# Kernel tuning notes

Measured on AMD Instinct MI355X. Metric: run time of the kernel, lower is better.

Reference implementation:

```python
import jax, jax.numpy as jnp
import numpy as np

N = 50000
E = 800000
IN_C = 64
HID = 64
OUT_C = 64


def setup_inputs() -> dict:
    key = jax.random.key(0)
    ks = jax.random.split(key, 16)
    s = lambda fan_in: 1.0 / np.sqrt(fan_in)
    inp = {
        "h": jax.random.normal(ks[0], (N, IN_C), jnp.float32),
        "pos": jax.random.normal(ks[1], (N, 3), jnp.float32),
        "edge_index": jax.random.randint(ks[2], (2, E), 0, N, jnp.int64),
        # edge_mlp: Linear(2*IN_C+1, HID), SiLU, Linear(HID, HID), SiLU
        "We1": jax.random.normal(ks[3], (2 * IN_C + 1, HID), jnp.float32) * s(2 * IN_C + 1),
        "be1": jnp.zeros((HID,), jnp.float32),
        "We2": jax.random.normal(ks[4], (HID, HID), jnp.float32) * s(HID),
        "be2": jnp.zeros((HID,), jnp.float32),
        # coord_mlp: Linear(HID, HID), SiLU, Linear(HID, 1) with tiny init (xavier gain 1e-3)
        "Wc1": jax.random.normal(ks[5], (HID, HID), jnp.float32) * s(HID),
        "bc1": jnp.zeros((HID,), jnp.float32),
        "Wc2": jax.random.normal(ks[6], (HID, 1), jnp.float32) * (0.001 * s(HID)),
        "bc2": jnp.zeros((1,), jnp.float32),
        # node_mlp: Linear(IN_C+HID, HID), SiLU, Linear(HID, OUT_C)
        "Wn1": jax.random.normal(ks[7], (IN_C + HID, HID), jnp.float32) * s(IN_C + HID),
        "bn1": jnp.zeros((HID,), jnp.float32),
        "Wn2": jax.random.normal(ks[8], (HID, OUT_C), jnp.float32) * s(HID),
        "bn2": jnp.zeros((OUT_C,), jnp.float32),
    }
    return inp


def reference(h, pos, edge_index, We1, be1, We2, be2, Wc1, bc1, Wc2, bc2, Wn1, bn1, Wn2, bn2):
    row, col = edge_index[0], edge_index[1]
    n = h.shape[0]
    rel_pos = pos[row] - pos[col]                      # [E,3]
    dist_sq = jnp.sum(rel_pos * rel_pos, axis=-1, keepdims=True)  # [E,1]
    edge_input = jnp.concatenate([h[row], h[col], dist_sq], axis=-1)  # [E, 2*in+1]
    m = jax.nn.silu(edge_input @ We1 + be1)
    edge_msg = jax.nn.silu(m @ We2 + be2)              # [E,HID]
    # coordinate update
    cw = jax.nn.silu(edge_msg @ Wc1 + bc1) @ Wc2 + bc2  # [E,1]
    coord_agg = jax.ops.segment_sum(rel_pos * cw, row, num_segments=n)  # [N,3]
    pos_out = pos + coord_agg
    # message aggregation + node update
    msg_agg = jax.ops.segment_sum(edge_msg, row, num_segments=n)  # [N,HID]
    node_input = jnp.concatenate([h, msg_agg], axis=-1)
    h_out = jax.nn.silu(node_input @ Wn1 + bn1) @ Wn2 + bn2  # [N,OUT_C]
    return h_out, pos_out
```

## Files before the change

### kernel.cpp

```cpp
#include <hip/hip_runtime.h>


#define NN 50000
#define NE 800000
#define ETILE 12500

#define SBLK 250
#define SCHUNK 3200
#define NBUK 196
#define GHN 64000
#define SCAN_NB 63

typedef __attribute__((ext_vector_type(8))) short bf16x8;
typedef __attribute__((ext_vector_type(4))) short bf16x4;
typedef __attribute__((ext_vector_type(4))) float f32x4;

#define MFMA16(a, b, c) __builtin_amdgcn_mfma_f32_16x16x32_bf16(a, b, c, 0, 0, 0)

__device__ __forceinline__ unsigned short f2b(float x) {
    union { float f; unsigned u; } v; v.f = x;
    return (unsigned short)((v.u + 0x8000u) >> 16);
}
__device__ __forceinline__ float b2f(unsigned short b) {
    union { unsigned u; float f; } v; v.u = ((unsigned)b) << 16; return v.f;
}
__device__ __forceinline__ float silu_f(float x) {
    return x * __builtin_amdgcn_rcpf(1.0f + __expf(-x));
}



#define P1_A 250
#define P1_FRAG 10
#define P1_NPRE 782
#define P1_ZERO 200
#define P1_COPY 16
#define P1_FRAG0 (P1_A)
#define P1_NPRE0 (P1_A + P1_FRAG)
#define P1_ZERO0 (P1_NPRE0 + P1_NPRE)
#define P1_COPY0 (P1_ZERO0 + P1_ZERO)
#define K1_GRID (P1_COPY0 + P1_COPY)

__global__ __launch_bounds__(256, 4) void prep_kernel(
    const float* __restrict__ h, const float* __restrict__ pos,
    const float* __restrict__ be1,
    const float* __restrict__ We1, const float* __restrict__ We2,
    const float* __restrict__ Wc1, const float* __restrict__ Wn1,
    const float* __restrict__ Wn2, const int* __restrict__ ei,
    unsigned short* __restrict__ wfrag, int* __restrict__ gh,
    unsigned short* __restrict__ a1r, unsigned short* __restrict__ a1c,
    float* __restrict__ msg_agg, float* __restrict__ pos_out,
    float4* __restrict__ pos4)
{
    __shared__ __align__(16) unsigned short sH[64][72];
    __shared__ __align__(16) unsigned short sT[4][16][72];
    __shared__ int lh[256];
    const int b = blockIdx.x, tid = threadIdx.x;
    if (b < P1_A) {
        lh[tid] = 0;
        __syncthreads();
        const int base = b * SCHUNK;
        for (int i = base + tid; i < base + SCHUNK; i += 256)
            atomicAdd(&lh[ei[i] >> 8], 1);
        __syncthreads();
        gh[tid * SBLK + b] = lh[tid];
    } else if (b < P1_NPRE0) {
        const int lane = tid & 63, w = tid >> 6;
        const int li = lane & 15, lg = lane >> 4;
        const int f = (b - P1_FRAG0) * 4 + w;
        const float* W; int g;
        if (f < 8)       { W = We2; g = f; }
        else if (f < 16) { W = Wc1; g = f - 8; }
        else if (f < 32) { W = Wn1; g = f - 16; }
        else             { W = Wn2; g = f - 32; }
        const int ks = g >> 2, ni = g & 3;
        const int n = ni * 16 + li, kb = ks * 32 + (lg << 3);
        bf16x8 v;
#pragma unroll
        for (int j = 0; j < 8; ++j) v[j] = (short)f2b(W[(kb + j) * 64 + n]);
        *(bf16x8*)(wfrag + (size_t)f * 512 + lane * 8) = v;
    } else if (b < P1_ZERO0) {
        const int lane = tid & 63, w = tid >> 6;
        const int li = lane & 15, lg = lane >> 4;
        const int t = b - P1_NPRE0;
        const int c4 = lane & 15, rsub = lane >> 4;
#pragma unroll
        for (int pass = 0; pass < 4; ++pass) {
            const int n_loc = w * 16 + pass * 4 + rsub;
            const int n = t * 64 + n_loc;
            float4 hv = make_float4(0.f, 0.f, 0.f, 0.f);
            if (n < NN) hv = *(const float4*)&h[(size_t)n * 64 + c4 * 4];
            bf16x4 hp;
            hp[0] = (short)f2b(hv.x); hp[1] = (short)f2b(hv.y);
            hp[2] = (short)f2b(hv.z); hp[3] = (short)f2b(hv.w);
            *(bf16x4*)&sH[n_loc][c4 * 4] = hp;
        }
        float be1v[4];
#pragma unroll
        for (int ni = 0; ni < 4; ++ni) be1v[ni] = be1[ni * 16 + li];

#pragma unroll
        for (int half = 0; half < 2; ++half) {
            unsigned short* out = half ? a1c : a1r;
            f32x4 acc[4];
#pragma unroll
            for (int ni = 0; ni < 4; ++ni) acc[ni] = (f32x4)(0.0f);
#pragma unroll
            for (int ks = 0; ks < 2; ++ks) {
                const bf16x8 afr = *(const bf16x8*)&sH[w * 16 + li][ks * 32 + (lg << 3)];
#pragma unroll
                for (int ni = 0; ni < 4; ++ni) {
                    const float* Wp = We1 +
                        (size_t)(half * 64 + ks * 32 + (lg << 3)) * 64 + ni * 16 + li;
                    bf16x8 bfr;
#pragma unroll
                    for (int j = 0; j < 8; ++j) bfr[j] = (short)f2b(Wp[(size_t)j * 64]);
                    acc[ni] = MFMA16(afr, bfr, acc[ni]);
                }
            }
#pragma unroll
            for (int ni = 0; ni < 4; ++ni)
#pragma unroll
                for (int reg = 0; reg < 4; ++reg)
                    sT[w][lg * 4 + reg][ni * 16 + li] =
                        f2b(acc[ni][reg] + (half ? 0.f : be1v[ni]));
#pragma unroll
            for (int pass = 0; pass < 2; ++pass) {
                const int rr = pass * 8 + (lane >> 3);
                const int n = t * 64 + w * 16 + rr;
                const bf16x8 v = *(const bf16x8*)&sT[w][rr][(lane & 7) * 8];
                if (n < NN) *(bf16x8*)&out[(size_t)n * 64 + (lane & 7) * 8] = v;
            }
        }
    } else if (b < P1_COPY0) {
        float4* dst = (float4*)msg_agg;
        int i = (b - P1_ZERO0) * 256 + tid;
        for (; i < NN * 16; i += P1_ZERO * 256) dst[i] = make_float4(0.f, 0.f, 0.f, 0.f);
    } else {
        if (b == P1_COPY0 && tid < 128) gh[GHN + tid] = 0;
        int i = (b - P1_COPY0) * 256 + tid;
        for (; i < 37500 + NN; i += P1_COPY * 256) {
            if (i < 37500) {
                ((float4*)pos_out)[i] = ((const float4*)pos)[i];
            } else {
                const int n = i - 37500;
                pos4[n] = make_float4(pos[3 * n], pos[3 * n + 1], pos[3 * n + 2], 0.f);
            }
        }
    }
}


__global__ __launch_bounds__(1024) void scan_kernel(int* __restrict__ cur,
                                                    int* __restrict__ aux) {
    __shared__ int wsum[16];
    __shared__ int s_prefix;
    const int b = blockIdx.x, t = threadIdx.x;
    const int g = b * 1024 + t;
    const int lane = t & 63, wid = t >> 6;
    const int v = (g < GHN) ? cur[g] : 0;
    int inc = v;
#pragma unroll
    for (int d = 1; d < 64; d <<= 1) {
        const int o = __shfl_up(inc, d, 64);
        if (lane >= d) inc += o;
    }
    if (lane == 63) wsum[wid] = inc;
    __syncthreads();
    if (t < 16) {
        int x = wsum[t];
#pragma unroll
        for (int d = 1; d < 16; d <<= 1) {
            const int o = __shfl_up(x, d, 16);
            if (t >= d) x += o;
        }
        wsum[t] = x;
    }
    __syncthreads();
    const int block_excl_w = (wid == 0) ? 0 : wsum[wid - 1];
    const int ex_in_block = block_excl_w + inc - v;
    if (t == 0) {
        __hip_atomic_store(&aux[b], wsum[15], __ATOMIC_RELAXED, __HIP_MEMORY_SCOPE_AGENT);
        __hip_atomic_store(&aux[SCAN_NB + b], 1, __ATOMIC_RELEASE, __HIP_MEMORY_SCOPE_AGENT);
    }
    if (t < 64) {
        int s = 0;
        if (t < b) {
            while (__hip_atomic_load(&aux[SCAN_NB + t], __ATOMIC_ACQUIRE,
                                     __HIP_MEMORY_SCOPE_AGENT) == 0) {
                __builtin_amdgcn_s_sleep(2);
            }
            s = __hip_atomic_load(&aux[t], __ATOMIC_RELAXED, __HIP_MEMORY_SCOPE_AGENT);
        }
#pragma unroll
        for (int m = 1; m < 64; m <<= 1) s += __shfl_xor(s, m, 64);
        if (t == 0) s_prefix = s;
    }
    __syncthreads();
    if (g < GHN) cur[g] = s_prefix + ex_in_block;
}


__global__ __launch_bounds__(256) void scat_kernel(const int* __restrict__ ei,
                                                   const int* __restrict__ gh,
                                                   int2* __restrict__ sorted_rc) {
    __shared__ int off[256];
    const int b = blockIdx.x, t = threadIdx.x;
    off[t] = gh[t * SBLK + b];
    __syncthreads();
    const int base = b * SCHUNK;
    for (int i = base + t; i < base + SCHUNK; i += 256) {
        const int r = ei[i];
        const int c = ei[NE + i];
        const int p = atomicAdd(&off[r >> 8], 1);
        sorted_rc[p] = make_int2(r, c);
    }
}


__global__ __launch_bounds__(256) void bsort_kernel(const int* __restrict__ gh,
                                                    int2* __restrict__ sorted_rc) {
    __shared__ int h2[256];
    __shared__ int sc[256];
    __shared__ int off2[256];
    __shared__ __align__(16) int2 stage[4096];
    const int k = blockIdx.x, t = threadIdx.x;
    const int start = gh[k * SBLK];
    const int end   = gh[(k + 1) * SBLK];
    for (int cb = start; cb < end; cb += 4096) {
        const int cnt = min(4096, end - cb);
        h2[t] = 0;
        __syncthreads();
        int2 le[16];
        int nloc = 0;
#pragma unroll
        for (int jj = 0; jj < 16; ++jj) {
            const int j = jj * 256 + t;
            if (j < cnt) {
                const int2 e = sorted_rc[cb + j];
                le[jj] = e;
                atomicAdd(&h2[e.x & 255], 1);
                nloc = jj + 1;
            }
        }
        __syncthreads();
        sc[t] = h2[t];
        __syncthreads();
        for (int d = 1; d < 256; d <<= 1) {
            const int v = (t >= d) ? sc[t - d] : 0;
            __syncthreads();
            sc[t] += v;
            __syncthreads();
        }
        off2[t] = sc[t] - h2[t];
        __syncthreads();
#pragma unroll
        for (int jj = 0; jj < 16; ++jj) {
            if (jj < nloc) {
                const int rank = atomicAdd(&off2[le[jj].x & 255], 1);
                stage[rank] = le[jj];
            }
        }
        __syncthreads();
        for (int j = t; j < cnt; j += 256) sorted_rc[cb + j] = stage[j];
        __syncthreads();
    }
}


__global__ __launch_bounds__(256, 6) void egnn_edge_kernel(
    const float4* __restrict__ pos4, const int2* __restrict__ sorted_rc,
    const unsigned short* __restrict__ a1r, const unsigned short* __restrict__ a1c,
    const float* __restrict__ We1,
    const unsigned short* __restrict__ wfrag,
    const float* __restrict__ be2, const float* __restrict__ bc1,
    const float* __restrict__ Wc2, const float* __restrict__ bc2,
    float* __restrict__ msg_agg, float* __restrict__ pos_out)
{
    __shared__ __align__(16) unsigned short sA[64][80];
    __shared__ __align__(8) int2 srce[64];
    __shared__ __align__(16) float4 sdr[64];
    __shared__ float scw[64];

    const int tid = threadIdx.x;
    const int lane = tid & 63, w = tid >> 6;
    const int li = lane & 15, lg = lane >> 4;
    const int tile = blockIdx.x;
    const int e0 = w * 16;

    if (lane < 16) {
        const int e = e0 + lane;
        const int2 rc = sorted_rc[tile * 64 + e];
        const float4 pr = pos4[rc.x];
        const float4 pc = pos4[rc.y];
        const float rx = pr.x - pc.x, ry = pr.y - pc.y, rz = pr.z - pc.z;
        srce[e] = rc;
        sdr[e] = make_float4(rx, ry, rz, rx * rx + ry * ry + rz * rz);
    }

    const int c8 = lane & 7;
    const int eo = lane >> 3;

    float w1d8[8];
    {
        const float* wd = We1 + 128 * 64 + c8 * 8;
        const float4 wa = *(const float4*)wd;
        const float4 wb = *(const float4*)(wd + 4);
        w1d8[0] = wa.x; w1d8[1] = wa.y; w1d8[2] = wa.z; w1d8[3] = wa.w;
        w1d8[4] = wb.x; w1d8[5] = wb.y; w1d8[6] = wb.z; w1d8[7] = wb.w;
    }
    float be2v[4], bc1v[4], wc2v[4];
#pragma unroll
    for (int ni = 0; ni < 4; ++ni) {
        be2v[ni] = be2[ni * 16 + li];
        bc1v[ni] = bc1[ni * 16 + li];
        wc2v[ni] = Wc2[ni * 16 + li];
    }
    const float bc2s = bc2[0];

#pragma unroll
    for (int hh = 0; hh < 2; ++hh) {
        const int e = e0 + hh * 8 + eo;
        const int2 rc = srce[e];
        const float dv = sdr[e].w;
        const bf16x8 ar = *(const bf16x8*)(a1r + (size_t)rc.x * 64 + c8 * 8);
        const bf16x8 ac = *(const bf16x8*)(a1c + (size_t)rc.y * 64 + c8 * 8);
        bf16x8 out;
#pragma unroll
        for (int j = 0; j < 8; ++j) {
            const float m = b2f((unsigned short)ar[j]) + b2f((unsigned short)ac[j])
                          + dv * w1d8[j];
            out[j] = (short)f2b(silu_f(m));
        }
        *(bf16x8*)&sA[e][c8 * 8] = out;
    }

    f32x4 acc[4];
#pragma unroll
    for (int ni = 0; ni < 4; ++ni) acc[ni] = (f32x4)(0.0f);
#pragma unroll
    for (int ks = 0; ks < 2; ++ks) {
        const bf16x8 af = *(const bf16x8*)&sA[e0 + li][ks * 32 + (lg << 3)];
#pragma unroll
        for (int ni = 0; ni < 4; ++ni) {
            const bf16x8 bf = *(const bf16x8*)(wfrag + (size_t)(ks * 4 + ni) * 512 + lane * 8);
            acc[ni] = MFMA16(af, bf, acc[ni]);
        }
    }

#pragma unroll
    for (int ni = 0; ni < 4; ++ni)
#pragma unroll
        for (int reg = 0; reg < 4; ++reg)
            sA[e0 + lg * 4 + reg][ni * 16 + li] = f2b(silu_f(acc[ni][reg] + be2v[ni]));

    {
        float macc = 0.0f;
        int pr = srce[e0].x;
#pragma unroll
        for (int j = 0; j < 16; ++j) {
            const int re = srce[e0 + j].x;
            if (re != pr) {
                atomicAdd(&msg_agg[(size_t)pr * 64 + lane], macc);
                macc = 0.0f;
                pr = re;
            }
            macc += b2f(sA[e0 + j][lane]);
        }
        atomicAdd(&msg_agg[(size_t)pr * 64 + lane], macc);
    }

    f32x4 a3[4];
#pragma unroll
    for (int ni = 0; ni < 4; ++ni) a3[ni] = (f32x4)(0.0f);
#pragma unroll
    for (int ks = 0; ks < 2; ++ks) {
        const bf16x8 af = *(const bf16x8*)&sA[e0 + li][ks * 32 + (lg << 3)];
#pragma unroll
        for (int ni = 0; ni < 4; ++ni) {
            const bf16x8 bf = *(const bf16x8*)(wfrag + (size_t)(8 + ks * 4 + ni) * 512 + lane * 8);
            a3[ni] = MFMA16(af, bf, a3[ni]);
        }
    }

    float sv[4];
#pragma unroll
    for (int reg = 0; reg < 4; ++reg) {
        float s = 0.0f;
#pragma unroll
        for (int ni = 0; ni < 4; ++ni)
            s += silu_f(a3[ni][reg] + bc1v[ni]) * wc2v[ni];
        sv[reg] = s;
    }
#pragma unroll
    for (int m = 1; m < 16; m <<= 1)
#pragma unroll
        for (int reg = 0; reg < 4; ++reg) sv[reg] += __shfl_xor(sv[reg], m, 64);
    if (li == 0) {
        float4 cv = make_float4(sv[0] + bc2s, sv[1] + bc2s, sv[2] + bc2s, sv[3] + bc2s);
        *(float4*)&scw[e0 + lg * 4] = cv;
    }
    __syncthreads();

    if (tid < 64) {
        const float4 dr = sdr[tid];
        const int r_e = srce[tid].x;
        const float cw = scw[tid];
        float vx = dr.x * cw, vy = dr.y * cw, vz = dr.z * cw;
#pragma unroll
        for (int d = 1; d < 64; d <<= 1) {
            const float ox = __shfl_up(vx, d, 64);
            const float oy = __shfl_up(vy, d, 64);
            const float oz = __shfl_up(vz, d, 64);
            const int   orr = __shfl_up(r_e, d, 64);
            const bool add = (tid >= d) && (orr == r_e);
            vx += add ? ox : 0.0f;
            vy += add ? oy : 0.0f;
            vz += add ? oz : 0.0f;
        }
        const int rnext = __shfl_down(r_e, 1, 64);
        const bool last = (tid == 63) || (rnext != r_e);
        if (last) {
            atomicAdd(&pos_out[r_e * 3 + 0], vx);
            atomicAdd(&pos_out[r_e * 3 + 1], vy);
            atomicAdd(&pos_out[r_e * 3 + 2], vz);
        }
    }
}


__global__ __launch_bounds__(256, 4) void node_kernel(
    const float* __restrict__ h, const float* __restrict__ msg_agg,
    const unsigned short* __restrict__ wfrag,
    const float* __restrict__ bn1, const float* __restrict__ bn2,
    float* __restrict__ h_out)
{
    __shared__ __align__(16) unsigned short sA[64][136];
    const int tid = threadIdx.x;
    const int lane = tid & 63, w = tid >> 6;
    const int t = blockIdx.x;
    const int li = lane & 15, lg = lane >> 4;

    float bn1v[4], bn2v[4];
#pragma unroll
    for (int ni = 0; ni < 4; ++ni) {
        bn1v[ni] = bn1[ni * 16 + li];
        bn2v[ni] = bn2[ni * 16 + li];
    }

#pragma unroll
    for (int pass = 0; pass < 8; ++pass) {
        const int idx = pass * 64 + lane;
        const int n_loc = w * 16 + (idx >> 5);
        const int c4 = idx & 31;
        const int n = t * 64 + n_loc;
        float4 v = make_float4(0.f, 0.f, 0.f, 0.f);
        if (n < NN) {
            const float* src = (c4 < 16) ? &h[(size_t)n * 64 + c4 * 4]
                                         : &msg_agg[(size_t)n * 64 + (c4 - 16) * 4];
            v = *(const float4*)src;
        }
        bf16x4 p;
        p[0] = (short)f2b(v.x); p[1] = (short)f2b(v.y);
        p[2] = (short)f2b(v.z); p[3] = (short)f2b(v.w);
        *(bf16x4*)&sA[n_loc][c4 * 4] = p;
    }

    f32x4 acc[4];
#pragma unroll
    for (int ni = 0; ni < 4; ++ni) acc[ni] = (f32x4)(0.0f);
#pragma unroll
    for (int ks = 0; ks < 4; ++ks) {
        const bf16x8 afr = *(const bf16x8*)&sA[w * 16 + li][ks * 32 + (lg << 3)];
#pragma unroll
        for (int ni = 0; ni < 4; ++ni) {
            const bf16x8 bfr = *(const bf16x8*)(wfrag + (size_t)(16 + ks * 4 + ni) * 512 + lane * 8);
            acc[ni] = MFMA16(afr, bfr, acc[ni]);
        }
    }
#pragma unroll
    for (int ni = 0; ni < 4; ++ni)
#pragma unroll
        for (int reg = 0; reg < 4; ++reg)
            sA[w * 16 + lg * 4 + reg][ni * 16 + li] = f2b(silu_f(acc[ni][reg] + bn1v[ni]));

    f32x4 a2[4];
#pragma unroll
    for (int ni = 0; ni < 4; ++ni) a2[ni] = (f32x4)(0.0f);
#pragma unroll
    for (int ks = 0; ks < 2; ++ks) {
        const bf16x8 afr = *(const bf16x8*)&sA[w * 16 + li][ks * 32 + (lg << 3)];
#pragma unroll
        for (int ni = 0; ni < 4; ++ni) {
            const bf16x8 bfr = *(const bf16x8*)(wfrag + (size_t)(32 + ks * 4 + ni) * 512 + lane * 8);
            a2[ni] = MFMA16(afr, bfr, a2[ni]);
        }
    }
#pragma unroll
    for (int ni = 0; ni < 4; ++ni)
#pragma unroll
        for (int reg = 0; reg < 4; ++reg) {
            const int n = t * 64 + w * 16 + lg * 4 + reg;
            if (n < NN) h_out[(size_t)n * 64 + ni * 16 + li] = a2[ni][reg] + bn2v[ni];
        }
}


extern "C" void kernel_launch(void* const* d_in, const int* in_sizes, int n_in,
                              void* d_out, int out_size, void* d_ws, size_t ws_size,
                              hipStream_t stream) {
    const float* h   = (const float*)d_in[0];
    const float* pos = (const float*)d_in[1];
    const int*   ei  = (const int*)d_in[2];
    const float* We1 = (const float*)d_in[3];
    const float* be1 = (const float*)d_in[4];
    const float* We2 = (const float*)d_in[5];
    const float* be2 = (const float*)d_in[6];
    const float* Wc1 = (const float*)d_in[7];
    const float* bc1 = (const float*)d_in[8];
    const float* Wc2 = (const float*)d_in[9];
    const float* bc2 = (const float*)d_in[10];
    const float* Wn1 = (const float*)d_in[11];
    const float* bn1 = (const float*)d_in[12];
    const float* Wn2 = (const float*)d_in[13];
    const float* bn2 = (const float*)d_in[14];

    unsigned short* a1r   = (unsigned short*)d_ws;
    unsigned short* a1c   = a1r + (size_t)NN * 64;
    unsigned short* wfrag = a1c + (size_t)NN * 64;
    int2* sorted_rc = (int2*)(wfrag + 40 * 512);
    int*  gh        = (int*)(sorted_rc + NE);
    float4* pos4    = (float4*)(gh + GHN + 128);

    float* msg_agg = (float*)d_out;
    float* pos_out = msg_agg + (size_t)NN * 64;

    prep_kernel<<<K1_GRID, 256, 0, stream>>>(h, pos, be1, We1, We2, Wc1, Wn1, Wn2,
                                             ei, wfrag, gh, a1r, a1c,
                                             msg_agg, pos_out, pos4);
    scan_kernel<<<SCAN_NB, 1024, 0, stream>>>(gh, gh + GHN);
    scat_kernel<<<SBLK, 256, 0, stream>>>(ei, gh, sorted_rc);
    bsort_kernel<<<NBUK, 256, 0, stream>>>(gh, sorted_rc);
    egnn_edge_kernel<<<ETILE, 256, 0, stream>>>(pos4, sorted_rc, a1r, a1c, We1, wfrag,
                                                be2, bc1, Wc2, bc2, msg_agg, pos_out);
    node_kernel<<<782, 256, 0, stream>>>(h, msg_agg, wfrag, bn1, bn2, msg_agg);
}
```

Measured before the change: 199.6 us.

## Fuse scan, scatter, bucket sort and node precompute into one kernel with flag sync

```diff
diff --git a/kernel.cpp b/kernel.cpp
--- a/kernel.cpp
+++ b/kernel.cpp
@@ -32,28 +32,22 @@
 
 #define P1_A 250
 #define P1_FRAG 10
-#define P1_NPRE 782
 #define P1_ZERO 200
 #define P1_COPY 16
 #define P1_FRAG0 (P1_A)
-#define P1_NPRE0 (P1_A + P1_FRAG)
-#define P1_ZERO0 (P1_NPRE0 + P1_NPRE)
+#define P1_ZERO0 (P1_FRAG0 + P1_FRAG)
 #define P1_COPY0 (P1_ZERO0 + P1_ZERO)
 #define K1_GRID (P1_COPY0 + P1_COPY)
 
 __global__ __launch_bounds__(256, 4) void prep_kernel(
-    const float* __restrict__ h, const float* __restrict__ pos,
-    const float* __restrict__ be1,
-    const float* __restrict__ We1, const float* __restrict__ We2,
-    const float* __restrict__ Wc1, const float* __restrict__ Wn1,
-    const float* __restrict__ Wn2, const int* __restrict__ ei,
+    const float* __restrict__ pos,
+    const float* __restrict__ We2, const float* __restrict__ Wc1,
+    const float* __restrict__ Wn1, const float* __restrict__ Wn2,
+    const int* __restrict__ ei,
     unsigned short* __restrict__ wfrag, int* __restrict__ gh,
-    unsigned short* __restrict__ a1r, unsigned short* __restrict__ a1c,
     float* __restrict__ msg_agg, float* __restrict__ pos_out,
     float4* __restrict__ pos4)
 {
-    __shared__ __align__(16) unsigned short sH[64][72];
-    __shared__ __align__(16) unsigned short sT[4][16][72];
     __shared__ int lh[256];
     const int b = blockIdx.x, tid = threadIdx.x;
     if (b < P1_A) {
@@ -64,7 +58,7 @@
             atomicAdd(&lh[ei[i] >> 8], 1);
         __syncthreads();
         gh[tid * SBLK + b] = lh[tid];
-    } else if (b < P1_NPRE0) {
+    } else if (b < P1_ZERO0) {
         const int lane = tid & 63, w = tid >> 6;
         const int li = lane & 15, lg = lane >> 4;
         const int f = (b - P1_FRAG0) * 4 + w;
@@ -79,59 +73,6 @@
 #pragma unroll
         for (int j = 0; j < 8; ++j) v[j] = (short)f2b(W[(kb + j) * 64 + n]);
         *(bf16x8*)(wfrag + (size_t)f * 512 + lane * 8) = v;
-    } else if (b < P1_ZERO0) {
-        const int lane = tid & 63, w = tid >> 6;
-        const int li = lane & 15, lg = lane >> 4;
-        const int t = b - P1_NPRE0;
-        const int c4 = lane & 15, rsub = lane >> 4;
-#pragma unroll
-        for (int pass = 0; pass < 4; ++pass) {
-            const int n_loc = w * 16 + pass * 4 + rsub;
-            const int n = t * 64 + n_loc;
-            float4 hv = make_float4(0.f, 0.f, 0.f, 0.f);
-            if (n < NN) hv = *(const float4*)&h[(size_t)n * 64 + c4 * 4];
-            bf16x4 hp;
-            hp[0] = (short)f2b(hv.x); hp[1] = (short)f2b(hv.y);
-            hp[2] = (short)f2b(hv.z); hp[3] = (short)f2b(hv.w);
-            *(bf16x4*)&sH[n_loc][c4 * 4] = hp;
-        }
-        float be1v[4];
-#pragma unroll
-        for (int ni = 0; ni < 4; ++ni) be1v[ni] = be1[ni * 16 + li];
-
-#pragma unroll
-        for (int half = 0; half < 2; ++half) {
-            unsigned short* out = half ? a1c : a1r;
-            f32x4 acc[4];
-#pragma unroll
-            for (int ni = 0; ni < 4; ++ni) acc[ni] = (f32x4)(0.0f);
-#pragma unroll
-            for (int ks = 0; ks < 2; ++ks) {
-                const bf16x8 afr = *(const bf16x8*)&sH[w * 16 + li][ks * 32 + (lg << 3)];
-#pragma unroll
-                for (int ni = 0; ni < 4; ++ni) {
-                    const float* Wp = We1 +
-                        (size_t)(half * 64 + ks * 32 + (lg << 3)) * 64 + ni * 16 + li;
-                    bf16x8 bfr;
-#pragma unroll
-                    for (int j = 0; j < 8; ++j) bfr[j] = (short)f2b(Wp[(size_t)j * 64]);
-                    acc[ni] = MFMA16(afr, bfr, acc[ni]);
-                }
-            }
-#pragma unroll
-            for (int ni = 0; ni < 4; ++ni)
-#pragma unroll
-                for (int reg = 0; reg < 4; ++reg)
-                    sT[w][lg * 4 + reg][ni * 16 + li] =
-                        f2b(acc[ni][reg] + (half ? 0.f : be1v[ni]));
-#pragma unroll
-            for (int pass = 0; pass < 2; ++pass) {
-                const int rr = pass * 8 + (lane >> 3);
-                const int n = t * 64 + w * 16 + rr;
-                const bf16x8 v = *(const bf16x8*)&sT[w][rr][(lane & 7) * 8];
-                if (n < NN) *(bf16x8*)&out[(size_t)n * 64 + (lane & 7) * 8] = v;
-            }
-        }
     } else if (b < P1_COPY0) {
         float4* dst = (float4*)msg_agg;
         int i = (b - P1_ZERO0) * 256 + tid;
@@ -151,119 +92,200 @@
 }
 
 
-__global__ __launch_bounds__(1024) void scan_kernel(int* __restrict__ cur,
-                                                    int* __restrict__ aux) {
-    __shared__ int wsum[16];
-    __shared__ int s_prefix;
-    const int b = blockIdx.x, t = threadIdx.x;
-    const int g = b * 1024 + t;
-    const int lane = t & 63, wid = t >> 6;
-    const int v = (g < GHN) ? cur[g] : 0;
-    int inc = v;
-#pragma unroll
-    for (int d = 1; d < 64; d <<= 1) {
-        const int o = __shfl_up(inc, d, 64);
-        if (lane >= d) inc += o;
-    }
-    if (lane == 63) wsum[wid] = inc;
-    __syncthreads();
-    if (t < 16) {
-        int x = wsum[t];
-#pragma unroll
-        for (int d = 1; d < 16; d <<= 1) {
-            const int o = __shfl_up(x, d, 16);
-            if (t >= d) x += o;
-        }
-        wsum[t] = x;
-    }
-    __syncthreads();
-    const int block_excl_w = (wid == 0) ? 0 : wsum[wid - 1];
-    const int ex_in_block = block_excl_w + inc - v;
-    if (t == 0) {
-        __hip_atomic_store(&aux[b], wsum[15], __ATOMIC_RELAXED, __HIP_MEMORY_SCOPE_AGENT);
-        __hip_atomic_store(&aux[SCAN_NB + b], 1, __ATOMIC_RELEASE, __HIP_MEMORY_SCOPE_AGENT);
-    }
-    if (t < 64) {
-        int s = 0;
-        if (t < b) {
-            while (__hip_atomic_load(&aux[SCAN_NB + t], __ATOMIC_ACQUIRE,
-                                     __HIP_MEMORY_SCOPE_AGENT) == 0) {
-                __builtin_amdgcn_s_sleep(2);
-            }
-            s = __hip_atomic_load(&aux[t], __ATOMIC_RELAXED, __HIP_MEMORY_SCOPE_AGENT);
-        }
-#pragma unroll
-        for (int m = 1; m < 64; m <<= 1) s += __shfl_xor(s, m, 64);
-        if (t == 0) s_prefix = s;
-    }
-    __syncthreads();
-    if (g < GHN) cur[g] = s_prefix + ex_in_block;
-}
-
-
-__global__ __launch_bounds__(256) void scat_kernel(const int* __restrict__ ei,
-                                                   const int* __restrict__ gh,
-                                                   int2* __restrict__ sorted_rc) {
-    __shared__ int off[256];
-    const int b = blockIdx.x, t = threadIdx.x;
-    off[t] = gh[t * SBLK + b];
-    __syncthreads();
-    const int base = b * SCHUNK;
-    for (int i = base + t; i < base + SCHUNK; i += 256) {
-        const int r = ei[i];
-        const int c = ei[NE + i];
-        const int p = atomicAdd(&off[r >> 8], 1);
-        sorted_rc[p] = make_int2(r, c);
-    }
-}
-
-
-__global__ __launch_bounds__(256) void bsort_kernel(const int* __restrict__ gh,
-                                                    int2* __restrict__ sorted_rc) {
-    __shared__ int h2[256];
-    __shared__ int sc[256];
-    __shared__ int off2[256];
-    __shared__ __align__(16) int2 stage[4096];
-    const int k = blockIdx.x, t = threadIdx.x;
-    const int start = gh[k * SBLK];
-    const int end   = gh[(k + 1) * SBLK];
-    for (int cb = start; cb < end; cb += 4096) {
-        const int cnt = min(4096, end - cb);
-        h2[t] = 0;
-        __syncthreads();
-        int2 le[16];
-        int nloc = 0;
-#pragma unroll
-        for (int jj = 0; jj < 16; ++jj) {
-            const int j = jj * 256 + t;
-            if (j < cnt) {
-                const int2 e = sorted_rc[cb + j];
-                le[jj] = e;
-                atomicAdd(&h2[e.x & 255], 1);
-                nloc = jj + 1;
-            }
-        }
-        __syncthreads();
-        sc[t] = h2[t];
-        __syncthreads();
-        for (int d = 1; d < 256; d <<= 1) {
-            const int v = (t >= d) ? sc[t - d] : 0;
+#define K2_SCAN 63
+#define K2_SCAT0 63
+#define K2_NPRE0 313
+#define K2_BS0 1095
+#define K2_GRID 1291
+
+union K2Smem {
+    struct { unsigned short sH[64][72]; unsigned short sT[4][16][72]; } np;
+    struct { int wsum[4]; int prefix; } scn;
+    struct { int off[256]; } st;
+    struct { int2 stage[4096]; int h2[256]; int sc2[256]; int off2[256]; } bs;
+};
+
+__global__ __launch_bounds__(256) void sort_fused_kernel(
+    const float* __restrict__ h, const float* __restrict__ be1,
+    const float* __restrict__ We1, const int* __restrict__ ei,
+    int* __restrict__ gh,
+    unsigned short* __restrict__ a1r, unsigned short* __restrict__ a1c,
+    int2* __restrict__ sorted_rc)
+{
+    __shared__ __align__(16) K2Smem smem;
+    const int b = blockIdx.x, tid = threadIdx.x;
+    int* aux = gh + GHN;
+    const int lane = tid & 63, wid = tid >> 6;
+
+    if (b < K2_SCAN) {
+        const int base4 = (b * 256 + tid) * 4;
+        int vv[4];
+#pragma unroll
+        for (int i = 0; i < 4; ++i) {
+            const int idx = base4 + i;
+            vv[i] = (idx < GHN) ? gh[idx] : 0;
+        }
+        const int s = vv[0] + vv[1] + vv[2] + vv[3];
+        int inc = s;
+#pragma unroll
+        for (int d = 1; d < 64; d <<= 1) {
+            const int o = __shfl_up(inc, d, 64);
+            if (lane >= d) inc += o;
+        }
+        if (lane == 63) smem.scn.wsum[wid] = inc;
+        __syncthreads();
+        if (tid == 0) {
+            int run = 0;
+#pragma unroll
+            for (int i = 0; i < 4; ++i) {
+                const int tmp = smem.scn.wsum[i]; smem.scn.wsum[i] = run; run += tmp;
+            }
+            __hip_atomic_store(&aux[b], run, __ATOMIC_RELAXED, __HIP_MEMORY_SCOPE_AGENT);
+            __hip_atomic_store(&aux[SCAN_NB + b], 1, __ATOMIC_RELEASE, __HIP_MEMORY_SCOPE_AGENT);
+        }
+        __syncthreads();
+        const int thr_excl = smem.scn.wsum[wid] + inc - s;
+        if (tid < 64) {
+            int s2 = 0;
+            if (tid < b) {
+                while (__hip_atomic_load(&aux[SCAN_NB + tid], __ATOMIC_ACQUIRE,
+                                         __HIP_MEMORY_SCOPE_AGENT) == 0) {
+                    __builtin_amdgcn_s_sleep(2);
+                }
+                s2 = __hip_atomic_load(&aux[tid], __ATOMIC_RELAXED, __HIP_MEMORY_SCOPE_AGENT);
+            }
+#pragma unroll
+            for (int m = 1; m < 64; m <<= 1) s2 += __shfl_xor(s2, m, 64);
+            if (tid == 0) smem.scn.prefix = s2;
+        }
+        __syncthreads();
+        int run = smem.scn.prefix + thr_excl;
+#pragma unroll
+        for (int i = 0; i < 4; ++i) {
+            const int idx = base4 + i;
+            if (idx < GHN) gh[idx] = run;
+            run += vv[i];
+        }
+        __syncthreads();
+        if (tid == 0)
+            __hip_atomic_fetch_add(&aux[126], 1, __ATOMIC_RELEASE, __HIP_MEMORY_SCOPE_AGENT);
+    } else if (b < K2_NPRE0) {
+        while (__hip_atomic_load(&aux[126], __ATOMIC_ACQUIRE,
+                                 __HIP_MEMORY_SCOPE_AGENT) != K2_SCAN) {
+            __builtin_amdgcn_s_sleep(2);
+        }
+        const int bb = b - K2_SCAT0;
+        smem.st.off[tid] = gh[tid * SBLK + bb];
+        __syncthreads();
+        const int base = bb * SCHUNK;
+        for (int i = base + tid; i < base + SCHUNK; i += 256) {
+            const int r = ei[i];
+            const int c = ei[NE + i];
+            const int p = atomicAdd(&smem.st.off[r >> 8], 1);
+            sorted_rc[p] = make_int2(r, c);
+        }
+        __syncthreads();
+        if (tid == 0)
+            __hip_atomic_fetch_add(&aux[127], 1, __ATOMIC_RELEASE, __HIP_MEMORY_SCOPE_AGENT);
+    } else if (b < K2_BS0) {
+        const int li = lane & 15, lg = lane >> 4;
+        const int w = wid;
+        const int t = b - K2_NPRE0;
+        const int c4 = lane & 15, rsub = lane >> 4;
+#pragma unroll
+        for (int pass = 0; pass < 4; ++pass) {
+            const int n_loc = w * 16 + pass * 4 + rsub;
+            const int n = t * 64 + n_loc;
+            float4 hv = make_float4(0.f, 0.f, 0.f, 0.f);
+            if (n < NN) hv = *(const float4*)&h[(size_t)n * 64 + c4 * 4];
+            bf16x4 hp;
+            hp[0] = (short)f2b(hv.x); hp[1] = (short)f2b(hv.y);
+            hp[2] = (short)f2b(hv.z); hp[3] = (short)f2b(hv.w);
+            *(bf16x4*)&smem.np.sH[n_loc][c4 * 4] = hp;
+        }
+        float be1v[4];
+#pragma unroll
+        for (int ni = 0; ni < 4; ++ni) be1v[ni] = be1[ni * 16 + li];
+
+#pragma unroll
+        for (int half = 0; half < 2; ++half) {
+            unsigned short* out = half ? a1c : a1r;
+            f32x4 acc[4];
+#pragma unroll
+            for (int ni = 0; ni < 4; ++ni) acc[ni] = (f32x4)(0.0f);
+#pragma unroll
+            for (int ks = 0; ks < 2; ++ks) {
+                const bf16x8 afr = *(const bf16x8*)&smem.np.sH[w * 16 + li][ks * 32 + (lg << 3)];
+#pragma unroll
+                for (int ni = 0; ni < 4; ++ni) {
+                    const float* Wp = We1 +
+                        (size_t)(half * 64 + ks * 32 + (lg << 3)) * 64 + ni * 16 + li;
+                    bf16x8 bfr;
+#pragma unroll
+                    for (int j = 0; j < 8; ++j) bfr[j] = (short)f2b(Wp[(size_t)j * 64]);
+                    acc[ni] = MFMA16(afr, bfr, acc[ni]);
+                }
+            }
+#pragma unroll
+            for (int ni = 0; ni < 4; ++ni)
+#pragma unroll
+                for (int reg = 0; reg < 4; ++reg)
+                    smem.np.sT[w][lg * 4 + reg][ni * 16 + li] =
+                        f2b(acc[ni][reg] + (half ? 0.f : be1v[ni]));
+#pragma unroll
+            for (int pass = 0; pass < 2; ++pass) {
+                const int rr = pass * 8 + (lane >> 3);
+                const int n = t * 64 + w * 16 + rr;
+                const bf16x8 v = *(const bf16x8*)&smem.np.sT[w][rr][(lane & 7) * 8];
+                if (n < NN) *(bf16x8*)&out[(size_t)n * 64 + (lane & 7) * 8] = v;
+            }
+        }
+    } else {
+        while (__hip_atomic_load(&aux[127], __ATOMIC_ACQUIRE,
+                                 __HIP_MEMORY_SCOPE_AGENT) != SBLK) {
+            __builtin_amdgcn_s_sleep(2);
+        }
+        const int k = b - K2_BS0, t = tid;
+        const int start = gh[k * SBLK];
+        const int end   = gh[(k + 1) * SBLK];
+        for (int cb = start; cb < end; cb += 4096) {
+            const int cnt = min(4096, end - cb);
+            smem.bs.h2[t] = 0;
             __syncthreads();
-            sc[t] += v;
+            int2 le[16];
+            int nloc = 0;
+#pragma unroll
+            for (int jj = 0; jj < 16; ++jj) {
+                const int j = jj * 256 + t;
+                if (j < cnt) {
+                    const int2 e = sorted_rc[cb + j];
+                    le[jj] = e;
+                    atomicAdd(&smem.bs.h2[e.x & 255], 1);
+                    nloc = jj + 1;
+                }
+            }
             __syncthreads();
-        }
-        off2[t] = sc[t] - h2[t];
-        __syncthreads();
-#pragma unroll
-        for (int jj = 0; jj < 16; ++jj) {
-            if (jj < nloc) {
-                const int rank = atomicAdd(&off2[le[jj].x & 255], 1);
-                stage[rank] = le[jj];
-            }
-        }
-        __syncthreads();
-        for (int j = t; j < cnt; j += 256) sorted_rc[cb + j] = stage[j];
-        __syncthreads();
+            smem.bs.sc2[t] = smem.bs.h2[t];
+            __syncthreads();
+            for (int d = 1; d < 256; d <<= 1) {
+                const int v = (t >= d) ? smem.bs.sc2[t - d] : 0;
+                __syncthreads();
+                smem.bs.sc2[t] += v;
+                __syncthreads();
+            }
+            smem.bs.off2[t] = smem.bs.sc2[t] - smem.bs.h2[t];
+            __syncthreads();
+#pragma unroll
+            for (int jj = 0; jj < 16; ++jj) {
+                if (jj < nloc) {
+                    const int rank = atomicAdd(&smem.bs.off2[le[jj].x & 255], 1);
+                    smem.bs.stage[rank] = le[jj];
+                }
+            }
+            __syncthreads();
+            for (int j = t; j < cnt; j += 256) sorted_rc[cb + j] = smem.bs.stage[j];
+            __syncthreads();
+        }
     }
 }
 
@@ -535,12 +557,10 @@
     float* msg_agg = (float*)d_out;
     float* pos_out = msg_agg + (size_t)NN * 64;
 
-    prep_kernel<<<K1_GRID, 256, 0, stream>>>(h, pos, be1, We1, We2, Wc1, Wn1, Wn2,
-                                             ei, wfrag, gh, a1r, a1c,
-                                             msg_agg, pos_out, pos4);
-    scan_kernel<<<SCAN_NB, 1024, 0, stream>>>(gh, gh + GHN);
-    scat_kernel<<<SBLK, 256, 0, stream>>>(ei, gh, sorted_rc);
-    bsort_kernel<<<NBUK, 256, 0, stream>>>(gh, sorted_rc);
+    prep_kernel<<<K1_GRID, 256, 0, stream>>>(pos, We2, Wc1, Wn1, Wn2, ei,
+                                             wfrag, gh, msg_agg, pos_out, pos4);
+    sort_fused_kernel<<<K2_GRID, 256, 0, stream>>>(h, be1, We1, ei, gh,
+                                                   a1r, a1c, sorted_rc);
     egnn_edge_kernel<<<ETILE, 256, 0, stream>>>(pos4, sorted_rc, a1r, a1c, We1, wfrag,
                                                 be2, bc1, Wc2, bc2, msg_agg, pos_out);
     node_kernel<<<782, 256, 0, stream>>>(h, msg_agg, wfrag, bn1, bn2, msg_agg);
```

New measurement: 401.4 us. 2.01x slower.

## Fuse scan and scatter kernels with device-wide flag sync; raise edge kernel occupancy

Applied to the files above, without the earlier changes.

```diff
diff --git a/kernel.cpp b/kernel.cpp
--- a/kernel.cpp
+++ b/kernel.cpp
@@ -151,69 +151,87 @@
 }
 
 
-__global__ __launch_bounds__(1024) void scan_kernel(int* __restrict__ cur,
-                                                    int* __restrict__ aux) {
-    __shared__ int wsum[16];
+#define SS_SCAN 63
+#define SS_GRID 313
+
+__global__ __launch_bounds__(256) void scanscat_kernel(
+    const int* __restrict__ ei, int* __restrict__ gh,
+    int2* __restrict__ sorted_rc)
+{
+    __shared__ int wsum[4];
     __shared__ int s_prefix;
-    const int b = blockIdx.x, t = threadIdx.x;
-    const int g = b * 1024 + t;
-    const int lane = t & 63, wid = t >> 6;
-    const int v = (g < GHN) ? cur[g] : 0;
-    int inc = v;
-#pragma unroll
-    for (int d = 1; d < 64; d <<= 1) {
-        const int o = __shfl_up(inc, d, 64);
-        if (lane >= d) inc += o;
-    }
-    if (lane == 63) wsum[wid] = inc;
-    __syncthreads();
-    if (t < 16) {
-        int x = wsum[t];
-#pragma unroll
-        for (int d = 1; d < 16; d <<= 1) {
-            const int o = __shfl_up(x, d, 16);
-            if (t >= d) x += o;
-        }
-        wsum[t] = x;
-    }
-    __syncthreads();
-    const int block_excl_w = (wid == 0) ? 0 : wsum[wid - 1];
-    const int ex_in_block = block_excl_w + inc - v;
-    if (t == 0) {
-        __hip_atomic_store(&aux[b], wsum[15], __ATOMIC_RELAXED, __HIP_MEMORY_SCOPE_AGENT);
-        __hip_atomic_store(&aux[SCAN_NB + b], 1, __ATOMIC_RELEASE, __HIP_MEMORY_SCOPE_AGENT);
-    }
-    if (t < 64) {
-        int s = 0;
-        if (t < b) {
-            while (__hip_atomic_load(&aux[SCAN_NB + t], __ATOMIC_ACQUIRE,
-                                     __HIP_MEMORY_SCOPE_AGENT) == 0) {
-                __builtin_amdgcn_s_sleep(2);
-            }
-            s = __hip_atomic_load(&aux[t], __ATOMIC_RELAXED, __HIP_MEMORY_SCOPE_AGENT);
-        }
-#pragma unroll
-        for (int m = 1; m < 64; m <<= 1) s += __shfl_xor(s, m, 64);
-        if (t == 0) s_prefix = s;
-    }
-    __syncthreads();
-    if (g < GHN) cur[g] = s_prefix + ex_in_block;
-}
-
-
-__global__ __launch_bounds__(256) void scat_kernel(const int* __restrict__ ei,
-                                                   const int* __restrict__ gh,
-                                                   int2* __restrict__ sorted_rc) {
     __shared__ int off[256];
-    const int b = blockIdx.x, t = threadIdx.x;
-    off[t] = gh[t * SBLK + b];
-    __syncthreads();
-    const int base = b * SCHUNK;
-    for (int i = base + t; i < base + SCHUNK; i += 256) {
-        const int r = ei[i];
-        const int c = ei[NE + i];
-        const int p = atomicAdd(&off[r >> 8], 1);
-        sorted_rc[p] = make_int2(r, c);
+    const int b = blockIdx.x, tid = threadIdx.x;
+    int* aux = gh + GHN;
+    const int lane = tid & 63, wid = tid >> 6;
+
+    if (b < SS_SCAN) {
+        const int base4 = (b * 256 + tid) * 4;
+        int vv[4];
+#pragma unroll
+        for (int i = 0; i < 4; ++i) {
+            const int idx = base4 + i;
+            vv[i] = (idx < GHN) ? gh[idx] : 0;
+        }
+        const int s = vv[0] + vv[1] + vv[2] + vv[3];
+        int inc = s;
+#pragma unroll
+        for (int d = 1; d < 64; d <<= 1) {
+            const int o = __shfl_up(inc, d, 64);
+            if (lane >= d) inc += o;
+        }
+        if (lane == 63) wsum[wid] = inc;
+        __syncthreads();
+        if (tid == 0) {
+            int run = 0;
+#pragma unroll
+            for (int i = 0; i < 4; ++i) {
+                const int tmp = wsum[i]; wsum[i] = run; run += tmp;
+            }
+            __hip_atomic_store(&aux[b], run, __ATOMIC_RELAXED, __HIP_MEMORY_SCOPE_AGENT);
+            __hip_atomic_store(&aux[SCAN_NB + b], 1, __ATOMIC_RELEASE, __HIP_MEMORY_SCOPE_AGENT);
+        }
+        __syncthreads();
+        const int thr_excl = wsum[wid] + inc - s;
+        if (tid < 64) {
+            int s2 = 0;
+            if (tid < b) {
+                while (__hip_atomic_load(&aux[SCAN_NB + tid], __ATOMIC_ACQUIRE,
+                                         __HIP_MEMORY_SCOPE_AGENT) == 0) {
+                    __builtin_amdgcn_s_sleep(2);
+                }
+                s2 = __hip_atomic_load(&aux[tid], __ATOMIC_RELAXED, __HIP_MEMORY_SCOPE_AGENT);
+            }
+#pragma unroll
+            for (int m = 1; m < 64; m <<= 1) s2 += __shfl_xor(s2, m, 64);
+            if (tid == 0) s_prefix = s2;
+        }
+        __syncthreads();
+        int run = s_prefix + thr_excl;
+#pragma unroll
+        for (int i = 0; i < 4; ++i) {
+            const int idx = base4 + i;
+            if (idx < GHN) gh[idx] = run;
+            run += vv[i];
+        }
+        __syncthreads();
+        if (tid == 0)
+            __hip_atomic_fetch_add(&aux[126], 1, __ATOMIC_RELEASE, __HIP_MEMORY_SCOPE_AGENT);
+    } else {
+        while (__hip_atomic_load(&aux[126], __ATOMIC_ACQUIRE,
+                                 __HIP_MEMORY_SCOPE_AGENT) != SS_SCAN) {
+            __builtin_amdgcn_s_sleep(2);
+        }
+        const int bb = b - SS_SCAN;
+        off[tid] = gh[tid * SBLK + bb];
+        __syncthreads();
+        const int base = bb * SCHUNK;
+        for (int i = base + tid; i < base + SCHUNK; i += 256) {
+            const int r = ei[i];
+            const int c = ei[NE + i];
+            const int p = atomicAdd(&off[r >> 8], 1);
+            sorted_rc[p] = make_int2(r, c);
+        }
     }
 }
 
@@ -268,7 +286,7 @@
 }
 
 
-__global__ __launch_bounds__(256, 6) void egnn_edge_kernel(
+__global__ __launch_bounds__(256, 8) void egnn_edge_kernel(
     const float4* __restrict__ pos4, const int2* __restrict__ sorted_rc,
     const unsigned short* __restrict__ a1r, const unsigned short* __restrict__ a1c,
     const float* __restrict__ We1,
@@ -538,8 +556,7 @@
     prep_kernel<<<K1_GRID, 256, 0, stream>>>(h, pos, be1, We1, We2, Wc1, Wn1, Wn2,
                                              ei, wfrag, gh, a1r, a1c,
                                              msg_agg, pos_out, pos4);
-    scan_kernel<<<SCAN_NB, 1024, 0, stream>>>(gh, gh + GHN);
-    scat_kernel<<<SBLK, 256, 0, stream>>>(ei, gh, sorted_rc);
+    scanscat_kernel<<<SS_GRID, 256, 0, stream>>>(ei, gh, sorted_rc);
     bsort_kernel<<<NBUK, 256, 0, stream>>>(gh, sorted_rc);
     egnn_edge_kernel<<<ETILE, 256, 0, stream>>>(pos4, sorted_rc, a1r, a1c, We1, wfrag,
                                                 be2, bc1, Wc2, bc2, msg_agg, pos_out);
```

Measured after the change: 263.1 us. +31.8%, slower.
